# Kernel tuning notes

Hardware: AMD Instinct MI355X
Metric: run time of the kernel (lower is better)

## Reference

```python
import jax, jax.numpy as jnp
import numpy as np
from jax.ops import segment_sum, segment_max

N, E, G = 50000, 800000, 64   # nodes, edges, graphs
H, C = 3, 64                   # heads, out channels per head
IN, ED = 75, 1                 # in feature dim, edge feature dim


def gat_conv(x, edge_index, edge_attr, W, a_src, a_dst, We, a_e, bias):
    """PyG GATConv (concat heads, self-loops with fill_value='mean', eval mode)."""
    n = x.shape[0]
    xh = (x @ W).reshape(n, H, C)                       # [n,H,C]
    src, dst = edge_index[0], edge_index[1]
    # self-loop edge_attr = mean of incoming edge_attr per node
    ones = jnp.ones((src.shape[0],), x.dtype)
    cnt = segment_sum(ones, dst, num_segments=n)
    loop_attr = segment_sum(edge_attr, dst, num_segments=n) / jnp.maximum(cnt, 1.0)[:, None]
    loops = jnp.arange(n)
    s = jnp.concatenate([src, loops])
    d = jnp.concatenate([dst, loops])
    ea = jnp.concatenate([edge_attr, loop_attr], axis=0)
    eh = (ea @ We).reshape(-1, H, C)                    # [E+n,H,C]
    asrc = (xh * a_src).sum(-1)                         # [n,H]
    adst = (xh * a_dst).sum(-1)
    alpha = asrc[s] + adst[d] + (eh * a_e).sum(-1)      # [E+n,H]
    alpha = jax.nn.leaky_relu(alpha, 0.2)
    # segment softmax over destination nodes
    amax = segment_max(alpha, d, num_segments=n)
    ex = jnp.exp(alpha - amax[d])
    denom = segment_sum(ex, d, num_segments=n)
    attn = ex / (denom[d] + 1e-16)                      # [E+n,H]
    out = segment_sum(xh[s] * attn[:, :, None], d, num_segments=n)
    return out.reshape(n, H * C) + bias, attn


def setup_inputs() -> dict:
    key = jax.random.key(0)
    ks = jax.random.split(key, 24)
    f = lambda k, sh, sc: (jax.random.normal(k, sh, jnp.float32) * sc)
    inp = {
        "x": f(ks[0], (N, IN), 1.0),
        "edge_attr": jax.random.uniform(ks[1], (E, ED), jnp.float32),
        "W1": f(ks[2], (IN, H * C), 0.1),
        "att_src1": f(ks[3], (H, C), 0.1),
        "att_dst1": f(ks[4], (H, C), 0.1),
        "We1": f(ks[5], (ED, H * C), 0.1),
        "att_e1": f(ks[6], (H, C), 0.1),
        "b1": f(ks[7], (H * C,), 0.1),
        "W2": f(ks[8], (H * C, H * C), 0.1),
        "att_src2": f(ks[9], (H, C), 0.1),
        "att_dst2": f(ks[10], (H, C), 0.1),
        "We2": f(ks[11], (ED, H * C), 0.1),
        "att_e2": f(ks[12], (H, C), 0.1),
        "b2": f(ks[13], (H * C,), 0.1),
        "fc1_w": f(ks[14], (H * C * 2, C), 0.1),
        "fc1_b": f(ks[15], (C,), 0.1),
        "fc2_w": f(ks[16], (C, 1), 0.1),
        "fc2_b": f(ks[17], (1,), 0.1),
        "edge_index": jax.random.randint(ks[18], (2, E), 0, N, jnp.int64),
        "batch": jnp.sort(jax.random.randint(ks[19], (N,), 0, G, jnp.int64)),
    }
    return inp


def reference(x, edge_attr, W1, att_src1, att_dst1, We1, att_e1, b1,
              W2, att_src2, att_dst2, We2, att_e2, b2,
              fc1_w, fc1_b, fc2_w, fc2_b, edge_index, batch):
    h, attn1 = gat_conv(x, edge_index, edge_attr, W1, att_src1, att_dst1, We1, att_e1, b1)
    h = jax.nn.elu(h)
    h, attn2 = gat_conv(h, edge_index, edge_attr, W2, att_src2, att_dst2, We2, att_e2, b2)
    h = jax.nn.elu(h)
    # global mean / max pooling over graphs
    cnt = segment_sum(jnp.ones((N,), h.dtype), batch, num_segments=G)
    x_mean = segment_sum(h, batch, num_segments=G) / jnp.maximum(cnt, 1.0)[:, None]
    x_max = segment_max(h, batch, num_segments=G)
    z = jnp.concatenate([x_mean, x_max], axis=1)        # [G, 2*H*C]
    z = jax.nn.relu(z @ fc1_w + fc1_b)
    logits = (z @ fc2_w + fc2_b)[:, 0]                  # [G]
    return logits, attn1, attn2
```

## Files before the change

kernel.cpp:

```cpp
#include <hip/hip_runtime.h>
#include <hip/hip_bf16.h>

typedef unsigned int u32;
typedef __attribute__((ext_vector_type(8))) short short8;
typedef __attribute__((ext_vector_type(4))) float f32x4;

#define NN 50000
#define NPAD 50048
#define EE 800000
#define GG 64
#define HH 3
#define CC 64
#define IN_DIM 75
#define KP1 96
#define HC 192
#define TOTAL (EE + NN)

__device__ __forceinline__ u32 fmap(float f) {
    u32 u = __float_as_uint(f);
    return (u & 0x80000000u) ? ~u : (u | 0x80000000u);
}
__device__ __forceinline__ float funmap(u32 m) {
    u32 u = (m & 0x80000000u) ? (m ^ 0x80000000u) : ~m;
    return __uint_as_float(u);
}

__global__ void k_deg(const int* __restrict__ ei, const float* __restrict__ eattr,
                      int* __restrict__ deg, float* __restrict__ attrsum) {
    int e = blockIdx.x * 256 + threadIdx.x;
    if (e >= EE) return;
    int d = ei[EE + e];
    atomicAdd(&deg[d], 1);
    atomicAdd(&attrsum[d], eattr[e]);
}

__global__ void k_scan1(const int* __restrict__ deg, u32* __restrict__ startv,
                        u32* __restrict__ blocksum) {
    __shared__ u32 sh[1024];
    int t = threadIdx.x;
    int n = blockIdx.x * 1024 + t;
    u32 v = (n < NN) ? (u32)(deg[n] + 1) : 0u;
    u32 val = v;
    sh[t] = val;
    __syncthreads();
    for (int off = 1; off < 1024; off <<= 1) {
        u32 y = (t >= off) ? sh[t - off] : 0u;
        __syncthreads();
        val += y;
        sh[t] = val;
        __syncthreads();
    }
    if (n < NN) startv[n] = val - v;
    if (t == 0) blocksum[blockIdx.x] = sh[1023];
}

__global__ void k_scan2(u32* __restrict__ blocksum, int nb) {
    if (threadIdx.x == 0) {
        u32 acc = 0;
        for (int b = 0; b < nb; b++) { u32 t = blocksum[b]; blocksum[b] = acc; acc += t; }
    }
}

__global__ void k_scan3(u32* __restrict__ startv, const u32* __restrict__ blocksum,
                        u32* __restrict__ cursor) {
    int n = blockIdx.x * 256 + threadIdx.x;
    if (n >= NN) return;
    u32 s = startv[n] + blocksum[n >> 10];
    startv[n] = s;
    cursor[n] = s;
}

__global__ void k_fill(const int* __restrict__ ei, const float* __restrict__ eattr,
                       const float* __restrict__ attrsum, const int* __restrict__ deg,
                       u32* __restrict__ cursor, int* __restrict__ srcP,
                       int* __restrict__ dstP, float* __restrict__ eaP,
                       u32* __restrict__ posOf) {
    int i = blockIdx.x * 256 + threadIdx.x;
    if (i >= TOTAL) return;
    int s, d;
    float ea;
    if (i < EE) {
        s = ei[i]; d = ei[EE + i]; ea = eattr[i];
    } else {
        s = d = i - EE;
        ea = attrsum[s] / fmaxf((float)deg[s], 1.f);
    }
    u32 pos = atomicAdd(&cursor[d], 1u);
    srcP[pos] = s;
    dstP[pos] = d;
    eaP[pos] = ea;
    posOf[i] = pos;
}

__global__ void k_wedot(const float* __restrict__ We1, const float* __restrict__ ae1,
                        const float* __restrict__ We2, const float* __restrict__ ae2,
                        float* __restrict__ wedot) {
    int w = threadIdx.x >> 6;
    int c = threadIdx.x & 63;
    int layer = w / 3, h = w % 3;
    const float* We = layer ? We2 : We1;
    const float* ae = layer ? ae2 : ae1;
    float v = We[h * 64 + c] * ae[h * 64 + c];
#pragma unroll
    for (int off = 32; off; off >>= 1) v += __shfl_xor(v, off, 64);
    if (c == 0) wedot[layer * 3 + h] = v;
}

__global__ void k_xconv(const float* __restrict__ x, __hip_bfloat16* __restrict__ xb) {
    int i = blockIdx.x * 256 + threadIdx.x;
    if (i >= NPAD * KP1) return;
    int n = i / KP1, k = i - n * KP1;
    float v = (n < NN && k < IN_DIM) ? x[n * IN_DIM + k] : 0.f;
    xb[i] = __float2bfloat16(v);
}

__global__ void k_wtconv(const float* __restrict__ W1, const float* __restrict__ W2,
                         __hip_bfloat16* __restrict__ Wt1, __hip_bfloat16* __restrict__ Wt2) {
    int i = blockIdx.x * 256 + threadIdx.x;
    if (i < HC * KP1) {
        int j = i / KP1, k = i - j * KP1;
        Wt1[i] = __float2bfloat16(k < IN_DIM ? W1[k * HC + j] : 0.f);
    }
    if (i < HC * HC) {
        int j = i / HC, k = i - j * HC;
        Wt2[i] = __float2bfloat16(W2[k * HC + j]);
    }
}

template <int KPAD>
__global__ __launch_bounds__(256) void k_mfma_gemm(const __hip_bfloat16* __restrict__ A,
                                                   const __hip_bfloat16* __restrict__ Wt,
                                                   float* __restrict__ out) {
    int wid = threadIdx.x >> 6;
    int lane = threadIdx.x & 63;
    int r0 = blockIdx.x * 64 + wid * 16;
    int lr = lane & 15;
    int g = lane >> 4;
    const short* Ab = (const short*)A;
    const short* Wb = (const short*)Wt;
    f32x4 acc[12];
#pragma unroll
    for (int f = 0; f < 12; f++) acc[f] = (f32x4){0.f, 0.f, 0.f, 0.f};
#pragma unroll
    for (int k0 = 0; k0 < KPAD; k0 += 32) {
        short8 a = *(const short8*)(Ab + (size_t)(r0 + lr) * KPAD + k0 + 8 * g);
#pragma unroll
        for (int f = 0; f < 12; f++) {
            short8 b = *(const short8*)(Wb + (size_t)(f * 16 + lr) * KPAD + k0 + 8 * g);
            acc[f] = __builtin_amdgcn_mfma_f32_16x16x32_bf16(a, b, acc[f], 0, 0, 0);
        }
    }
    int rbase = r0 + 4 * g;
#pragma unroll
    for (int f = 0; f < 12; f++) {
        int col = f * 16 + lr;
#pragma unroll
        for (int r = 0; r < 4; r++) {
            int row = rbase + r;
            if (row < NN) out[(size_t)row * HC + col] = acc[f][r];
        }
    }
}

__global__ void k_attdot(const float* __restrict__ xh, const float* __restrict__ asrcw,
                         const float* __restrict__ adstw, float* __restrict__ asrc,
                         float* __restrict__ adst) {
    int n = blockIdx.x;
    int h = threadIdx.x >> 6, c = threadIdx.x & 63;
    float v = xh[(size_t)n * HC + h * 64 + c];
    float p = v * asrcw[h * 64 + c];
    float q = v * adstw[h * 64 + c];
#pragma unroll
    for (int off = 32; off; off >>= 1) {
        p += __shfl_xor(p, off, 64);
        q += __shfl_xor(q, off, 64);
    }
    if (c == 0) { asrc[n * 3 + h] = p; adst[n * 3 + h] = q; }
}

__global__ void k_alphaP(const int* __restrict__ srcP, const int* __restrict__ dstP,
                         const float* __restrict__ eaP, const float* __restrict__ asrc,
                         const float* __restrict__ adst, const float* __restrict__ wedot,
                         int woff, float* __restrict__ alphaP) {
    int p = blockIdx.x * 256 + threadIdx.x;
    if (p >= TOTAL) return;
    int s = srcP[p], d = dstP[p];
    float ea = eaP[p];
#pragma unroll
    for (int h = 0; h < 3; h++) {
        float a = asrc[s * 3 + h] + adst[d * 3 + h] + ea * wedot[woff + h];
        alphaP[(size_t)p * 3 + h] = (a > 0.f) ? a : 0.2f * a;
    }
}

template <int OUT_BF16>
__global__ void k_gatherSM(const u32* __restrict__ startv, const int* __restrict__ deg,
                           const int* __restrict__ srcP, float* __restrict__ alphaP,
                           const float* __restrict__ xh, const float* __restrict__ bias,
                           float* __restrict__ rdenom, float* __restrict__ hout,
                           __hip_bfloat16* __restrict__ hb) {
    int n = blockIdx.x;
    int j = threadIdx.x;
    int h = j >> 6;
    u32 st = startv[n];
    int L = deg[n] + 1;
    const float* ap = alphaP + (size_t)st * 3 + h;
    const int* sp = srcP + st;

    float m = -1e30f;
    int p = 0;
    for (; p + 4 <= L; p += 4) {
        float a0 = ap[3 * p], a1 = ap[3 * p + 3], a2 = ap[3 * p + 6], a3 = ap[3 * p + 9];
        m = fmaxf(m, fmaxf(fmaxf(a0, a1), fmaxf(a2, a3)));
    }
    for (; p < L; p++) m = fmaxf(m, ap[3 * p]);

    float acc = 0.f, ssum = 0.f;
    int c = j & 63;
    p = 0;
    for (; p + 4 <= L; p += 4) {
        int s0 = sp[p], s1 = sp[p + 1], s2 = sp[p + 2], s3 = sp[p + 3];
        float e0 = __expf(ap[3 * p] - m);
        float e1 = __expf(ap[3 * p + 3] - m);
        float e2 = __expf(ap[3 * p + 6] - m);
        float e3 = __expf(ap[3 * p + 9] - m);
        float x0 = xh[(size_t)s0 * HC + j];
        float x1 = xh[(size_t)s1 * HC + j];
        float x2 = xh[(size_t)s2 * HC + j];
        float x3 = xh[(size_t)s3 * HC + j];
        if (c == 0) {
            alphaP[(size_t)(st + p) * 3 + h] = e0;
            alphaP[(size_t)(st + p + 1) * 3 + h] = e1;
            alphaP[(size_t)(st + p + 2) * 3 + h] = e2;
            alphaP[(size_t)(st + p + 3) * 3 + h] = e3;
        }
        acc += e0 * x0;
        acc += e1 * x1;
        acc += e2 * x2;
        acc += e3 * x3;
        ssum += (e0 + e1) + (e2 + e3);
    }
    for (; p < L; p++) {
        int s0 = sp[p];
        float e0 = __expf(ap[3 * p] - m);
        float x0 = xh[(size_t)s0 * HC + j];
        if (c == 0) alphaP[(size_t)(st + p) * 3 + h] = e0;
        acc += e0 * x0;
        ssum += e0;
    }
    float r = 1.f / (ssum + 1e-16f);
    if (c == 0) rdenom[n * 3 + h] = r;
    float o = acc * r + bias[j];
    o = (o > 0.f) ? o : expm1f(o);
    if (OUT_BF16) hb[(size_t)n * HC + j] = __float2bfloat16(o);
    else hout[(size_t)n * HC + j] = o;
}

__global__ void k_attnout(const u32* __restrict__ posOf, const int* __restrict__ ei,
                          const float* __restrict__ eP, const float* __restrict__ rdenom,
                          float* __restrict__ attn) {
    int i = blockIdx.x * 256 + threadIdx.x;
    if (i >= TOTAL) return;
    u32 pos = posOf[i];
    int d = (i < EE) ? ei[EE + i] : (i - EE);
#pragma unroll
    for (int h = 0; h < 3; h++)
        attn[(size_t)i * 3 + h] = eP[(size_t)pos * 3 + h] * rdenom[d * 3 + h];
}

__global__ void k_poolinit(u32* __restrict__ pmax) {
    int i = blockIdx.x * 256 + threadIdx.x;
    if (i < GG * HC) pmax[i] = 0x007FFFFFu;
}

__global__ void k_pool(const float* __restrict__ h2, const int* __restrict__ batch,
                       float* __restrict__ psum, u32* __restrict__ pmax,
                       int* __restrict__ pcnt) {
    const int CH = 256;
    int n0 = blockIdx.x * CH;
    if (n0 >= NN) return;
    int j = threadIdx.x;
    int nend = min(NN, n0 + CH);
    int curg = batch[n0];
    float sum = 0.f, mx = -1e30f;
    int c = 0;
    for (int n = n0; n < nend; n++) {
        int g = batch[n];
        if (g != curg) {
            atomicAdd(&psum[curg * HC + j], sum);
            atomicMax(&pmax[curg * HC + j], fmap(mx));
            if (j == 0) atomicAdd(&pcnt[curg], c);
            sum = 0.f; mx = -1e30f; c = 0; curg = g;
        }
        float v = h2[(size_t)n * HC + j];
        sum += v;
        mx = fmaxf(mx, v);
        c++;
    }
    atomicAdd(&psum[curg * HC + j], sum);
    atomicMax(&pmax[curg * HC + j], fmap(mx));
    if (j == 0) atomicAdd(&pcnt[curg], c);
}

__global__ void k_head(const float* __restrict__ psum, const u32* __restrict__ pmax,
                       const int* __restrict__ pcnt, const float* __restrict__ fc1w,
                       const float* __restrict__ fc1b, const float* __restrict__ fc2w,
                       const float* __restrict__ fc2b, float* __restrict__ logits) {
    __shared__ float z[2 * HC];
    int g = blockIdx.x;
    int t = threadIdx.x;
    float cnt = fmaxf((float)pcnt[g], 1.f);
    for (int k = t; k < 2 * HC; k += 64)
        z[k] = (k < HC) ? psum[g * HC + k] / cnt : funmap(pmax[g * HC + (k - HC)]);
    __syncthreads();
    float acc = fc1b[t];
    for (int k = 0; k < 2 * HC; k++) acc += z[k] * fc1w[k * 64 + t];
    acc = fmaxf(acc, 0.f);
    float v = acc * fc2w[t];
#pragma unroll
    for (int off = 32; off; off >>= 1) v += __shfl_xor(v, off, 64);
    if (t == 0) logits[g] = v + fc2b[0];
}

extern "C" void kernel_launch(void* const* d_in, const int* in_sizes, int n_in,
                              void* d_out, int out_size, void* d_ws, size_t ws_size,
                              hipStream_t stream) {
    const float* x     = (const float*)d_in[0];
    const float* eattr = (const float*)d_in[1];
    const float* W1    = (const float*)d_in[2];
    const float* as1   = (const float*)d_in[3];
    const float* ad1   = (const float*)d_in[4];
    const float* We1   = (const float*)d_in[5];
    const float* ae1   = (const float*)d_in[6];
    const float* b1    = (const float*)d_in[7];
    const float* W2    = (const float*)d_in[8];
    const float* as2   = (const float*)d_in[9];
    const float* ad2   = (const float*)d_in[10];
    const float* We2   = (const float*)d_in[11];
    const float* ae2   = (const float*)d_in[12];
    const float* b2    = (const float*)d_in[13];
    const float* fc1w  = (const float*)d_in[14];
    const float* fc1b  = (const float*)d_in[15];
    const float* fc2w  = (const float*)d_in[16];
    const float* fc2b  = (const float*)d_in[17];
    const int* ei      = (const int*)d_in[18];
    const int* batch   = (const int*)d_in[19];

    float* logits = (float*)d_out;
    float* attn1  = logits + GG;
    float* attn2  = attn1 + (size_t)TOTAL * 3;

    float* bufA    = (float*)d_ws;
    float* bufB    = bufA + (size_t)NN * HC;
    float* alphaP  = bufB + (size_t)NN * HC;
    int*   srcP    = (int*)(alphaP + (size_t)TOTAL * 3);
    int*   dstP    = srcP + TOTAL;
    float* eaP     = (float*)(dstP + TOTAL);
    u32*   posOf   = (u32*)(eaP + TOTAL);
    int*   deg     = (int*)(posOf + TOTAL);
    float* attrsum = (float*)(deg + NN);
    float* asrc    = attrsum + NN;
    float* adst    = asrc + NN * 3;
    float* rdenom  = adst + NN * 3;
    u32*   startv  = (u32*)(rdenom + NN * 3);
    u32*   cursor  = startv + NN;
    u32*   blocksum= cursor + NN;
    float* wedot   = (float*)(blocksum + 64);
    float* psum    = wedot + 8;
    u32*   pmax    = (u32*)(psum + GG * HC);
    int*   pcnt    = (int*)(pmax + GG * HC);
    __hip_bfloat16* xb  = (__hip_bfloat16*)(pcnt + 64);
    __hip_bfloat16* hb  = xb + (size_t)NPAD * KP1;
    __hip_bfloat16* Wt1 = hb + (size_t)NPAD * HC;
    __hip_bfloat16* Wt2 = Wt1 + (size_t)HC * KP1;

    hipMemsetAsync(deg, 0, NN * sizeof(int), stream);
    hipMemsetAsync(attrsum, 0, NN * sizeof(float), stream);
    hipMemsetAsync(psum, 0, GG * HC * sizeof(float), stream);
    hipMemsetAsync(pcnt, 0, GG * sizeof(int), stream);
    hipMemsetAsync(hb + (size_t)NN * HC, 0, (size_t)(NPAD - NN) * HC * sizeof(__hip_bfloat16), stream);

    k_deg<<<(EE + 255) / 256, 256, 0, stream>>>(ei, eattr, deg, attrsum);
    k_scan1<<<49, 1024, 0, stream>>>(deg, startv, blocksum);
    k_scan2<<<1, 64, 0, stream>>>(blocksum, 49);
    k_scan3<<<(NN + 255) / 256, 256, 0, stream>>>(startv, blocksum, cursor);
    k_fill<<<(TOTAL + 255) / 256, 256, 0, stream>>>(ei, eattr, attrsum, deg, cursor,
                                                    srcP, dstP, eaP, posOf);
    k_wedot<<<1, 384, 0, stream>>>(We1, ae1, We2, ae2, wedot);
    k_poolinit<<<(GG * HC + 255) / 256, 256, 0, stream>>>(pmax);
    k_xconv<<<(NPAD * KP1 + 255) / 256, 256, 0, stream>>>(x, xb);
    k_wtconv<<<(HC * HC + 255) / 256, 256, 0, stream>>>(W1, W2, Wt1, Wt2);

    const int GB = NPAD / 64;

    k_mfma_gemm<KP1><<<GB, 256, 0, stream>>>(xb, Wt1, bufA);
    k_attdot<<<NN, 192, 0, stream>>>(bufA, as1, ad1, asrc, adst);
    k_alphaP<<<(TOTAL + 255) / 256, 256, 0, stream>>>(srcP, dstP, eaP, asrc, adst,
                                                      wedot, 0, alphaP);
    k_gatherSM<1><<<NN, 192, 0, stream>>>(startv, deg, srcP, alphaP, bufA, b1, rdenom,
                                          bufB, hb);
    k_attnout<<<(TOTAL + 255) / 256, 256, 0, stream>>>(posOf, ei, alphaP, rdenom, attn1);

    k_mfma_gemm<HC><<<GB, 256, 0, stream>>>(hb, Wt2, bufA);
    k_attdot<<<NN, 192, 0, stream>>>(bufA, as2, ad2, asrc, adst);
    k_alphaP<<<(TOTAL + 255) / 256, 256, 0, stream>>>(srcP, dstP, eaP, asrc, adst,
                                                      wedot, 3, alphaP);
    k_gatherSM<0><<<NN, 192, 0, stream>>>(startv, deg, srcP, alphaP, bufA, b2, rdenom,
                                          bufB, hb);
    k_attnout<<<(TOTAL + 255) / 256, 256, 0, stream>>>(posOf, ei, alphaP, rdenom, attn2);

    k_pool<<<(NN + 255) / 256, 192, 0, stream>>>(bufB, batch, psum, pmax, pcnt);
    k_head<<<GG, 64, 0, stream>>>(psum, pmax, pcnt, fc1w, fc1b, fc2w, fc2b, logits);
}
```

Baseline: 772.0 us.

## Fuse attention dots into GEMM epilogue and alpha/pooling into gather kernel

The per-node attention dot products are computed in the MFMA GEMM epilogue with cross-lane shuffles, replacing the separate attdot kernel. Edge logits are computed directly inside the gather softmax, which drops the alphaP kernel and the separate max pass; exp is taken without subtracting the per-node maximum. Mean and max pooling move into the layer-2 gather through per-node global atomics, and node counts move into scan3. Small prep kernels are merged, and attnout now reads in CSR order and scatters its writes. This cuts kernel launches and intermediate traffic, but risks exp overflow and heavy atomic contention on the 64 pooled graph rows.

```diff
diff --git a/kernel.cpp b/kernel.cpp
--- a/kernel.cpp
+++ b/kernel.cpp
@@ -62,19 +62,21 @@
 }
 
 __global__ void k_scan3(u32* __restrict__ startv, const u32* __restrict__ blocksum,
-                        u32* __restrict__ cursor) {
+                        u32* __restrict__ cursor, const int* __restrict__ batch,
+                        int* __restrict__ pcnt) {
     int n = blockIdx.x * 256 + threadIdx.x;
     if (n >= NN) return;
     u32 s = startv[n] + blocksum[n >> 10];
     startv[n] = s;
     cursor[n] = s;
+    atomicAdd(&pcnt[batch[n]], 1);
 }
 
 __global__ void k_fill(const int* __restrict__ ei, const float* __restrict__ eattr,
                        const float* __restrict__ attrsum, const int* __restrict__ deg,
                        u32* __restrict__ cursor, int* __restrict__ srcP,
                        int* __restrict__ dstP, float* __restrict__ eaP,
-                       u32* __restrict__ posOf) {
+                       u32* __restrict__ iOf) {
     int i = blockIdx.x * 256 + threadIdx.x;
     if (i >= TOTAL) return;
     int s, d;
@@ -89,21 +91,36 @@
     srcP[pos] = s;
     dstP[pos] = d;
     eaP[pos] = ea;
-    posOf[i] = pos;
-}
-
-__global__ void k_wedot(const float* __restrict__ We1, const float* __restrict__ ae1,
-                        const float* __restrict__ We2, const float* __restrict__ ae2,
-                        float* __restrict__ wedot) {
-    int w = threadIdx.x >> 6;
-    int c = threadIdx.x & 63;
-    int layer = w / 3, h = w % 3;
-    const float* We = layer ? We2 : We1;
-    const float* ae = layer ? ae2 : ae1;
-    float v = We[h * 64 + c] * ae[h * 64 + c];
-#pragma unroll
-    for (int off = 32; off; off >>= 1) v += __shfl_xor(v, off, 64);
-    if (c == 0) wedot[layer * 3 + h] = v;
+    iOf[pos] = (u32)i;
+}
+
+__global__ void k_prep(const float* __restrict__ W1, const float* __restrict__ W2,
+                       const float* __restrict__ We1, const float* __restrict__ ae1,
+                       const float* __restrict__ We2, const float* __restrict__ ae2,
+                       __hip_bfloat16* __restrict__ Wt1, __hip_bfloat16* __restrict__ Wt2,
+                       u32* __restrict__ pmax, float* __restrict__ wedot) {
+    int i = blockIdx.x * 256 + threadIdx.x;
+    if (i < HC * KP1) {
+        int j = i / KP1, k = i - j * KP1;
+        Wt1[i] = __float2bfloat16(k < IN_DIM ? W1[k * HC + j] : 0.f);
+    }
+    if (i < HC * HC) {
+        int j = i / HC, k = i - j * HC;
+        Wt2[i] = __float2bfloat16(W2[k * HC + j]);
+    }
+    if (i < GG * HC) pmax[i] = 0x007FFFFFu;
+    if (blockIdx.x == 0) {
+        int w = threadIdx.x >> 6, c = threadIdx.x & 63;
+        for (int dd = w; dd < 6; dd += 4) {
+            int layer = dd / 3, h = dd - 3 * layer;
+            const float* We = layer ? We2 : We1;
+            const float* ae = layer ? ae2 : ae1;
+            float v = We[h * 64 + c] * ae[h * 64 + c];
+#pragma unroll
+            for (int off = 32; off; off >>= 1) v += __shfl_xor(v, off, 64);
+            if (c == 0) wedot[dd] = v;
+        }
+    }
 }
 
 __global__ void k_xconv(const float* __restrict__ x, __hip_bfloat16* __restrict__ xb) {
@@ -114,23 +131,14 @@
     xb[i] = __float2bfloat16(v);
 }
 
-__global__ void k_wtconv(const float* __restrict__ W1, const float* __restrict__ W2,
-                         __hip_bfloat16* __restrict__ Wt1, __hip_bfloat16* __restrict__ Wt2) {
-    int i = blockIdx.x * 256 + threadIdx.x;
-    if (i < HC * KP1) {
-        int j = i / KP1, k = i - j * KP1;
-        Wt1[i] = __float2bfloat16(k < IN_DIM ? W1[k * HC + j] : 0.f);
-    }
-    if (i < HC * HC) {
-        int j = i / HC, k = i - j * HC;
-        Wt2[i] = __float2bfloat16(W2[k * HC + j]);
-    }
-}
-
 template <int KPAD>
 __global__ __launch_bounds__(256) void k_mfma_gemm(const __hip_bfloat16* __restrict__ A,
                                                    const __hip_bfloat16* __restrict__ Wt,
-                                                   float* __restrict__ out) {
+                                                   const float* __restrict__ asrcw,
+                                                   const float* __restrict__ adstw,
+                                                   float* __restrict__ out,
+                                                   float* __restrict__ asrc,
+                                                   float* __restrict__ adst) {
     int wid = threadIdx.x >> 6;
     int lane = threadIdx.x & 63;
     int r0 = blockIdx.x * 64 + wid * 16;
@@ -160,79 +168,77 @@
             if (row < NN) out[(size_t)row * HC + col] = acc[f][r];
         }
     }
-}
-
-__global__ void k_attdot(const float* __restrict__ xh, const float* __restrict__ asrcw,
-                         const float* __restrict__ adstw, float* __restrict__ asrc,
-                         float* __restrict__ adst) {
-    int n = blockIdx.x;
-    int h = threadIdx.x >> 6, c = threadIdx.x & 63;
-    float v = xh[(size_t)n * HC + h * 64 + c];
-    float p = v * asrcw[h * 64 + c];
-    float q = v * adstw[h * 64 + c];
-#pragma unroll
-    for (int off = 32; off; off >>= 1) {
-        p += __shfl_xor(p, off, 64);
-        q += __shfl_xor(q, off, 64);
-    }
-    if (c == 0) { asrc[n * 3 + h] = p; adst[n * 3 + h] = q; }
-}
-
-__global__ void k_alphaP(const int* __restrict__ srcP, const int* __restrict__ dstP,
-                         const float* __restrict__ eaP, const float* __restrict__ asrc,
-                         const float* __restrict__ adst, const float* __restrict__ wedot,
-                         int woff, float* __restrict__ alphaP) {
-    int p = blockIdx.x * 256 + threadIdx.x;
-    if (p >= TOTAL) return;
-    int s = srcP[p], d = dstP[p];
-    float ea = eaP[p];
+    float asw[12], adw[12];
+#pragma unroll
+    for (int f = 0; f < 12; f++) {
+        asw[f] = asrcw[f * 16 + lr];
+        adw[f] = adstw[f * 16 + lr];
+    }
 #pragma unroll
     for (int h = 0; h < 3; h++) {
-        float a = asrc[s * 3 + h] + adst[d * 3 + h] + ea * wedot[woff + h];
-        alphaP[(size_t)p * 3 + h] = (a > 0.f) ? a : 0.2f * a;
-    }
-}
-
-template <int OUT_BF16>
+#pragma unroll
+        for (int r = 0; r < 4; r++) {
+            float p = acc[4 * h][r] * asw[4 * h] + acc[4 * h + 1][r] * asw[4 * h + 1] +
+                      acc[4 * h + 2][r] * asw[4 * h + 2] + acc[4 * h + 3][r] * asw[4 * h + 3];
+            float q = acc[4 * h][r] * adw[4 * h] + acc[4 * h + 1][r] * adw[4 * h + 1] +
+                      acc[4 * h + 2][r] * adw[4 * h + 2] + acc[4 * h + 3][r] * adw[4 * h + 3];
+#pragma unroll
+            for (int off = 1; off < 16; off <<= 1) {
+                p += __shfl_xor(p, off, 64);
+                q += __shfl_xor(q, off, 64);
+            }
+            int row = rbase + r;
+            if (lr == 0 && row < NN) {
+                asrc[row * 3 + h] = p;
+                adst[row * 3 + h] = q;
+            }
+        }
+    }
+}
+
+template <int LAYER2>
 __global__ void k_gatherSM(const u32* __restrict__ startv, const int* __restrict__ deg,
-                           const int* __restrict__ srcP, float* __restrict__ alphaP,
-                           const float* __restrict__ xh, const float* __restrict__ bias,
-                           float* __restrict__ rdenom, float* __restrict__ hout,
-                           __hip_bfloat16* __restrict__ hb) {
+                           const int* __restrict__ srcP, const float* __restrict__ eaP,
+                           const float* __restrict__ asrc, const float* __restrict__ adst,
+                           const float* __restrict__ wedot, int woff,
+                           float* __restrict__ eP, const float* __restrict__ xh,
+                           const float* __restrict__ bias, float* __restrict__ rdenom,
+                           __hip_bfloat16* __restrict__ hb, const int* __restrict__ batch,
+                           float* __restrict__ psum, u32* __restrict__ pmax) {
     int n = blockIdx.x;
     int j = threadIdx.x;
-    int h = j >> 6;
+    int h = j >> 6, c = j & 63;
     u32 st = startv[n];
     int L = deg[n] + 1;
-    const float* ap = alphaP + (size_t)st * 3 + h;
+    float wd = wedot[woff + h];
+    float adx = adst[n * 3 + h];
     const int* sp = srcP + st;
-
-    float m = -1e30f;
+    const float* ep = eaP + st;
+    float* eo = eP + (size_t)st * 3 + h;
+
+    float acc = 0.f, ssum = 0.f;
     int p = 0;
     for (; p + 4 <= L; p += 4) {
-        float a0 = ap[3 * p], a1 = ap[3 * p + 3], a2 = ap[3 * p + 6], a3 = ap[3 * p + 9];
-        m = fmaxf(m, fmaxf(fmaxf(a0, a1), fmaxf(a2, a3)));
-    }
-    for (; p < L; p++) m = fmaxf(m, ap[3 * p]);
-
-    float acc = 0.f, ssum = 0.f;
-    int c = j & 63;
-    p = 0;
-    for (; p + 4 <= L; p += 4) {
         int s0 = sp[p], s1 = sp[p + 1], s2 = sp[p + 2], s3 = sp[p + 3];
-        float e0 = __expf(ap[3 * p] - m);
-        float e1 = __expf(ap[3 * p + 3] - m);
-        float e2 = __expf(ap[3 * p + 6] - m);
-        float e3 = __expf(ap[3 * p + 9] - m);
+        float ea0 = ep[p], ea1 = ep[p + 1], ea2 = ep[p + 2], ea3 = ep[p + 3];
+        float a0 = asrc[s0 * 3 + h] + adx + ea0 * wd;
+        float a1 = asrc[s1 * 3 + h] + adx + ea1 * wd;
+        float a2 = asrc[s2 * 3 + h] + adx + ea2 * wd;
+        float a3 = asrc[s3 * 3 + h] + adx + ea3 * wd;
+        a0 = (a0 > 0.f) ? a0 : 0.2f * a0;
+        a1 = (a1 > 0.f) ? a1 : 0.2f * a1;
+        a2 = (a2 > 0.f) ? a2 : 0.2f * a2;
+        a3 = (a3 > 0.f) ? a3 : 0.2f * a3;
+        float e0 = __expf(a0), e1 = __expf(a1), e2 = __expf(a2), e3 = __expf(a3);
         float x0 = xh[(size_t)s0 * HC + j];
         float x1 = xh[(size_t)s1 * HC + j];
         float x2 = xh[(size_t)s2 * HC + j];
         float x3 = xh[(size_t)s3 * HC + j];
         if (c == 0) {
-            alphaP[(size_t)(st + p) * 3 + h] = e0;
-            alphaP[(size_t)(st + p + 1) * 3 + h] = e1;
-            alphaP[(size_t)(st + p + 2) * 3 + h] = e2;
-            alphaP[(size_t)(st + p + 3) * 3 + h] = e3;
+            eo[3 * p] = e0;
+            eo[3 * (p + 1)] = e1;
+            eo[3 * (p + 2)] = e2;
+            eo[3 * (p + 3)] = e3;
         }
         acc += e0 * x0;
         acc += e1 * x1;
@@ -242,9 +248,11 @@
     }
     for (; p < L; p++) {
         int s0 = sp[p];
-        float e0 = __expf(ap[3 * p] - m);
+        float a0 = asrc[s0 * 3 + h] + adx + ep[p] * wd;
+        a0 = (a0 > 0.f) ? a0 : 0.2f * a0;
+        float e0 = __expf(a0);
         float x0 = xh[(size_t)s0 * HC + j];
-        if (c == 0) alphaP[(size_t)(st + p) * 3 + h] = e0;
+        if (c == 0) eo[3 * p] = e0;
         acc += e0 * x0;
         ssum += e0;
     }
@@ -252,54 +260,28 @@
     if (c == 0) rdenom[n * 3 + h] = r;
     float o = acc * r + bias[j];
     o = (o > 0.f) ? o : expm1f(o);
-    if (OUT_BF16) hb[(size_t)n * HC + j] = __float2bfloat16(o);
-    else hout[(size_t)n * HC + j] = o;
-}
-
-__global__ void k_attnout(const u32* __restrict__ posOf, const int* __restrict__ ei,
+    if (LAYER2) {
+        int gi = batch[n];
+        atomicAdd(&psum[gi * HC + j], o);
+        atomicMax(&pmax[gi * HC + j], fmap(o));
+    } else {
+        hb[(size_t)n * HC + j] = __float2bfloat16(o);
+    }
+}
+
+__global__ void k_attnout(const u32* __restrict__ iOf, const int* __restrict__ dstP,
                           const float* __restrict__ eP, const float* __restrict__ rdenom,
                           float* __restrict__ attn) {
-    int i = blockIdx.x * 256 + threadIdx.x;
-    if (i >= TOTAL) return;
-    u32 pos = posOf[i];
-    int d = (i < EE) ? ei[EE + i] : (i - EE);
-#pragma unroll
-    for (int h = 0; h < 3; h++)
-        attn[(size_t)i * 3 + h] = eP[(size_t)pos * 3 + h] * rdenom[d * 3 + h];
-}
-
-__global__ void k_poolinit(u32* __restrict__ pmax) {
-    int i = blockIdx.x * 256 + threadIdx.x;
-    if (i < GG * HC) pmax[i] = 0x007FFFFFu;
-}
-
-__global__ void k_pool(const float* __restrict__ h2, const int* __restrict__ batch,
-                       float* __restrict__ psum, u32* __restrict__ pmax,
-                       int* __restrict__ pcnt) {
-    const int CH = 256;
-    int n0 = blockIdx.x * CH;
-    if (n0 >= NN) return;
-    int j = threadIdx.x;
-    int nend = min(NN, n0 + CH);
-    int curg = batch[n0];
-    float sum = 0.f, mx = -1e30f;
-    int c = 0;
-    for (int n = n0; n < nend; n++) {
-        int g = batch[n];
-        if (g != curg) {
-            atomicAdd(&psum[curg * HC + j], sum);
-            atomicMax(&pmax[curg * HC + j], fmap(mx));
-            if (j == 0) atomicAdd(&pcnt[curg], c);
-            sum = 0.f; mx = -1e30f; c = 0; curg = g;
-        }
-        float v = h2[(size_t)n * HC + j];
-        sum += v;
-        mx = fmaxf(mx, v);
-        c++;
-    }
-    atomicAdd(&psum[curg * HC + j], sum);
-    atomicMax(&pmax[curg * HC + j], fmap(mx));
-    if (j == 0) atomicAdd(&pcnt[curg], c);
+    int pos = blockIdx.x * 256 + threadIdx.x;
+    if (pos >= TOTAL) return;
+    int d = dstP[pos];
+    u32 i = iOf[pos];
+    float e0 = eP[(size_t)pos * 3 + 0];
+    float e1 = eP[(size_t)pos * 3 + 1];
+    float e2 = eP[(size_t)pos * 3 + 2];
+    attn[(size_t)i * 3 + 0] = e0 * rdenom[d * 3 + 0];
+    attn[(size_t)i * 3 + 1] = e1 * rdenom[d * 3 + 1];
+    attn[(size_t)i * 3 + 2] = e2 * rdenom[d * 3 + 2];
 }
 
 __global__ void k_head(const float* __restrict__ psum, const u32* __restrict__ pmax,
@@ -351,13 +333,12 @@
     float* attn2  = attn1 + (size_t)TOTAL * 3;
 
     float* bufA    = (float*)d_ws;
-    float* bufB    = bufA + (size_t)NN * HC;
-    float* alphaP  = bufB + (size_t)NN * HC;
-    int*   srcP    = (int*)(alphaP + (size_t)TOTAL * 3);
+    float* eP      = bufA + (size_t)NN * HC;
+    int*   srcP    = (int*)(eP + (size_t)TOTAL * 3);
     int*   dstP    = srcP + TOTAL;
     float* eaP     = (float*)(dstP + TOTAL);
-    u32*   posOf   = (u32*)(eaP + TOTAL);
-    int*   deg     = (int*)(posOf + TOTAL);
+    u32*   iOf     = (u32*)(eaP + TOTAL);
+    int*   deg     = (int*)(iOf + TOTAL);
     float* attrsum = (float*)(deg + NN);
     float* asrc    = attrsum + NN;
     float* adst    = asrc + NN * 3;
@@ -383,32 +364,24 @@
     k_deg<<<(EE + 255) / 256, 256, 0, stream>>>(ei, eattr, deg, attrsum);
     k_scan1<<<49, 1024, 0, stream>>>(deg, startv, blocksum);
     k_scan2<<<1, 64, 0, stream>>>(blocksum, 49);
-    k_scan3<<<(NN + 255) / 256, 256, 0, stream>>>(startv, blocksum, cursor);
+    k_scan3<<<(NN + 255) / 256, 256, 0, stream>>>(startv, blocksum, cursor, batch, pcnt);
     k_fill<<<(TOTAL + 255) / 256, 256, 0, stream>>>(ei, eattr, attrsum, deg, cursor,
-                                                    srcP, dstP, eaP, posOf);
-    k_wedot<<<1, 384, 0, stream>>>(We1, ae1, We2, ae2, wedot);
-    k_poolinit<<<(GG * HC + 255) / 256, 256, 0, stream>>>(pmax);
+                                                    srcP, dstP, eaP, iOf);
+    k_prep<<<(HC * HC + 255) / 256, 256, 0, stream>>>(W1, W2, We1, ae1, We2, ae2,
+                                                      Wt1, Wt2, pmax, wedot);
     k_xconv<<<(NPAD * KP1 + 255) / 256, 256, 0, stream>>>(x, xb);
-    k_wtconv<<<(HC * HC + 255) / 256, 256, 0, stream>>>(W1, W2, Wt1, Wt2);
 
     const int GB = NPAD / 64;
 
-    k_mfma_gemm<KP1><<<GB, 256, 0, stream>>>(xb, Wt1, bufA);
-    k_attdot<<<NN, 192, 0, stream>>>(bufA, as1, ad1, asrc, adst);
-    k_alphaP<<<(TOTAL + 255) / 256, 256, 0, stream>>>(srcP, dstP, eaP, asrc, adst,
-                                                      wedot, 0, alphaP);
-    k_gatherSM<1><<<NN, 192, 0, stream>>>(startv, deg, srcP, alphaP, bufA, b1, rdenom,
-                                          bufB, hb);
-    k_attnout<<<(TOTAL + 255) / 256, 256, 0, stream>>>(posOf, ei, alphaP, rdenom, attn1);
-
-    k_mfma_gemm<HC><<<GB, 256, 0, stream>>>(hb, Wt2, bufA);
-    k_attdot<<<NN, 192, 0, stream>>>(bufA, as2, ad2, asrc, adst);
-    k_alphaP<<<(TOTAL + 255) / 256, 256, 0, stream>>>(srcP, dstP, eaP, asrc, adst,
-                                                      wedot, 3, alphaP);
-    k_gatherSM<0><<<NN, 192, 0, stream>>>(startv, deg, srcP, alphaP, bufA, b2, rdenom,
-                                          bufB, hb);
-    k_attnout<<<(TOTAL + 255) / 256, 256, 0, stream>>>(posOf, ei, alphaP, rdenom, attn2);
-
-    k_pool<<<(NN + 255) / 256, 192, 0, stream>>>(bufB, batch, psum, pmax, pcnt);
+    k_mfma_gemm<KP1><<<GB, 256, 0, stream>>>(xb, Wt1, as1, ad1, bufA, asrc, adst);
+    k_gatherSM<0><<<NN, 192, 0, stream>>>(startv, deg, srcP, eaP, asrc, adst, wedot, 0,
+                                          eP, bufA, b1, rdenom, hb, batch, psum, pmax);
+    k_attnout<<<(TOTAL + 255) / 256, 256, 0, stream>>>(iOf, dstP, eP, rdenom, attn1);
+
+    k_mfma_gemm<HC><<<GB, 256, 0, stream>>>(hb, Wt2, as2, ad2, bufA, asrc, adst);
+    k_gatherSM<1><<<NN, 192, 0, stream>>>(startv, deg, srcP, eaP, asrc, adst, wedot, 3,
+                                          eP, bufA, b2, rdenom, hb, batch, psum, pmax);
+    k_attnout<<<(TOTAL + 255) / 256, 256, 0, stream>>>(iOf, dstP, eP, rdenom, attn2);
+
     k_head<<<GG, 64, 0, stream>>>(psum, pmax, pcnt, fc1w, fc1b, fc2w, fc2b, logits);
 }
```

New measurement: 946.9 us. 1.23x slower.
